# Performance work log

Hardware: AMD Instinct MI355X
Metric: run time of the kernel (lower is better)

## Reference

```python
import jax, jax.numpy as jnp
import numpy as np

KH, KW = 3, 3      # kernel_size
SH, SW = 1, 1      # stride
MINVAL, MAXVAL = -0.45, -0.15


def setup_inputs() -> dict:
    key = jax.random.key(0)
    kx, kw = jax.random.split(key)
    x = jax.random.normal(kx, (16, 128, 128, 16), dtype=jnp.float32)  # NHWC
    W = jax.random.uniform(kw, (KH, KW, 16, 32), minval=MINVAL, maxval=MAXVAL,
                           dtype=jnp.float32)  # [kh, kw, C_in, filters]
    return {"x": x, "W": W}


def _dilation(x, W):
    # Max-plus sliding-window 'convolution' (VALID padding):
    # out[b,i,j,f] = max_{di,dj,c} x[b, i*SH+di, j*SW+dj, c] + W[di,dj,c,f]
    kh, kw, C, F = W.shape
    B, H, Wd, _ = x.shape
    Hout = (H - kh) // SH + 1
    Wout = (Wd - kw) // SW + 1
    out = jnp.full((B, Hout, Wout, F), -jnp.inf, dtype=x.dtype)
    for di in range(kh):          # small fixed loop over kernel offsets
        for dj in range(kw):
            xs = x[:, di:di + Hout * SH:SH, dj:dj + Wout * SW:SW, :]  # [B,Hout,Wout,C]
            # add W for this offset, reduce max over input channels
            out = jnp.maximum(out, jnp.max(xs[..., :, None] + W[di, dj], axis=3))
    return out


def reference(x, W):
    # erosion(x) = -dilation(-x)
    return -_dilation(-x, W)
```

## Files before the change

kernel.cpp:

```cpp
#include <hip/hip_runtime.h>
#include <math.h>


#define TI 21

typedef _Float16 h2 __attribute__((ext_vector_type(2)));

__device__ __forceinline__ h2 hmin2(h2 a, h2 b) {
    return __builtin_elementwise_min(a, b);
}

__device__ __forceinline__ h2 pkrtz(float a, float b) {
    auto r = __builtin_amdgcn_cvt_pkrtz(a, b);
    return *reinterpret_cast<h2*>(&r);
}

__device__ __forceinline__ h2 rowmin(const h2* hx, const h2 w[3][4]) {
    h2 t[12];
#pragma unroll
    for (int dj = 0; dj < 3; ++dj)
#pragma unroll
        for (int q = 0; q < 4; ++q)
            t[dj * 4 + q] = hx[dj * 4 + q] - w[dj][q];
#pragma unroll
    for (int k = 0; k < 6; ++k) t[k] = hmin2(t[k], t[k + 6]);
    t[0] = hmin2(t[0], t[3]);
    t[1] = hmin2(t[1], t[4]);
    t[2] = hmin2(t[2], t[5]);
    return hmin2(hmin2(t[0], t[1]), t[2]);
}

__global__ __launch_bounds__(256) void erosion_kernel(
    const float* __restrict__ x, const float* __restrict__ Wt,
    float* __restrict__ out)
{
    const int tid = threadIdx.x;
    const int f  = tid & 31;
    const int ch = (tid >> 5) & 1;
    const int jt = tid >> 6;
    const int b  = blockIdx.z;
    const int i0 = blockIdx.y * TI;
    int j = blockIdx.x * 4 + jt;
    const bool jvalid = (j < 126);
    if (!jvalid) j = 125;

    h2 wh[3][3][4];
#pragma unroll
    for (int di = 0; di < 3; ++di)
#pragma unroll
        for (int dj = 0; dj < 3; ++dj)
#pragma unroll
            for (int q = 0; q < 4; ++q) {
                int p = di * 3 + dj;
                float a = Wt[(p * 16 + ch * 8 + 2 * q) * 32 + f];
                float c = Wt[(p * 16 + ch * 8 + 2 * q + 1) * 32 + f];
                wh[di][dj][q] = pkrtz(a, c);
            }

    const float* xb = x + ((size_t)b * 128 * 128 + (size_t)j) * 16 + ch * 8;
    float* op = out + (((size_t)b * 126 + i0) * 126 + j) * 32 + f;

    const _Float16 HINF = (_Float16)__builtin_huge_valf();
    h2 accB = {HINF, HINF};
    h2 accC = {HINF, HINF};

#pragma unroll 1
    for (int r = 0; r < TI + 2; ++r) {
        const float* xr = xb + (size_t)(i0 + r) * 2048;
        h2 hx[12];
#pragma unroll
        for (int dj = 0; dj < 3; ++dj) {
            float4 lo = *reinterpret_cast<const float4*>(xr + dj * 16);
            float4 hi = *reinterpret_cast<const float4*>(xr + dj * 16 + 4);
            hx[dj * 4 + 0] = pkrtz(lo.x, lo.y);
            hx[dj * 4 + 1] = pkrtz(lo.z, lo.w);
            hx[dj * 4 + 2] = pkrtz(hi.x, hi.y);
            hx[dj * 4 + 3] = pkrtz(hi.z, hi.w);
        }

        h2 n0 = rowmin(hx, wh[0]);
        h2 n1 = rowmin(hx, wh[1]);
        h2 n2 = rowmin(hx, wh[2]);

        h2 fin2 = hmin2(accC, n2);
        accC = hmin2(accB, n1);
        accB = n0;

        if (r >= 2) {
            float v = fminf((float)fin2[0], (float)fin2[1]);
            v = fminf(v, __shfl_xor(v, 32));
            if (jvalid && ch == 0)
                op[(size_t)(r - 2) * (126 * 32)] = v;
        }
    }
}

extern "C" void kernel_launch(void* const* d_in, const int* in_sizes, int n_in,
                              void* d_out, int out_size, void* d_ws, size_t ws_size,
                              hipStream_t stream) {
    const float* x  = (const float*)d_in[0];
    const float* Wt = (const float*)d_in[1];
    float* out = (float*)d_out;

    dim3 grid(32, 6, 16);
    dim3 block(256);
    erosion_kernel<<<grid, block, 0, stream>>>(x, Wt, out);
}
```

Before: 129.6 us.

## Pre-convert input to fp16 in workspace before the erosion kernel

Adds a conversion kernel that writes x as fp16 into the workspace, and an erosion kernel that reads fp16 rows, which halves the bytes loaded per row and removes the per-load conversions. The main loop is unrolled by 2 in both kernels, and the final lane reduction is done in fp16 before widening. The cost is an extra launch plus a full pass that reads x and writes the fp16 copy, and the fast path runs only if the workspace is large enough.

```diff
diff --git a/kernel.cpp b/kernel.cpp
--- a/kernel.cpp
+++ b/kernel.cpp
@@ -28,6 +28,81 @@
     t[1] = hmin2(t[1], t[4]);
     t[2] = hmin2(t[2], t[5]);
     return hmin2(hmin2(t[0], t[1]), t[2]);
+}
+
+__global__ __launch_bounds__(256) void cvt_kernel(const float* __restrict__ x,
+                                                  _Float16* __restrict__ xh) {
+    int idx = (blockIdx.x * 256 + threadIdx.x) * 8;
+    float4 a = *reinterpret_cast<const float4*>(x + idx);
+    float4 b = *reinterpret_cast<const float4*>(x + idx + 4);
+    h2 o[4] = { pkrtz(a.x, a.y), pkrtz(a.z, a.w), pkrtz(b.x, b.y), pkrtz(b.z, b.w) };
+    *reinterpret_cast<float4*>(xh + idx) = *reinterpret_cast<float4*>(o);
+}
+
+__global__ __launch_bounds__(256) void erosion_h_kernel(
+    const _Float16* __restrict__ xh, const float* __restrict__ Wt,
+    float* __restrict__ out)
+{
+    const int tid = threadIdx.x;
+    const int f  = tid & 31;
+    const int ch = (tid >> 5) & 1;
+    const int jt = tid >> 6;
+    const int b  = blockIdx.z;
+    const int i0 = blockIdx.y * TI;
+    int j = blockIdx.x * 4 + jt;
+    const bool jvalid = (j < 126);
+    if (!jvalid) j = 125;
+
+    h2 wh[3][3][4];
+#pragma unroll
+    for (int di = 0; di < 3; ++di)
+#pragma unroll
+        for (int dj = 0; dj < 3; ++dj)
+#pragma unroll
+            for (int q = 0; q < 4; ++q) {
+                int p = di * 3 + dj;
+                float a = Wt[(p * 16 + ch * 8 + 2 * q) * 32 + f];
+                float c = Wt[(p * 16 + ch * 8 + 2 * q + 1) * 32 + f];
+                wh[di][dj][q] = pkrtz(a, c);
+            }
+
+    const _Float16* xb = xh + ((size_t)b * 128 * 128 + (size_t)j) * 16 + ch * 8;
+    float* op = out + (((size_t)b * 126 + i0) * 126 + j) * 32 + f;
+
+    const _Float16 HINF = (_Float16)__builtin_huge_valf();
+    h2 accB = {HINF, HINF};
+    h2 accC = {HINF, HINF};
+
+#pragma unroll 2
+    for (int r = 0; r < TI + 2; ++r) {
+        const _Float16* xr = xb + (size_t)(i0 + r) * 2048;
+        h2 hx[12];
+#pragma unroll
+        for (int dj = 0; dj < 3; ++dj) {
+            float4 raw = *reinterpret_cast<const float4*>(xr + dj * 16);
+            const h2* p = reinterpret_cast<const h2*>(&raw);
+            hx[dj * 4 + 0] = p[0];
+            hx[dj * 4 + 1] = p[1];
+            hx[dj * 4 + 2] = p[2];
+            hx[dj * 4 + 3] = p[3];
+        }
+
+        h2 n0 = rowmin(hx, wh[0]);
+        h2 n1 = rowmin(hx, wh[1]);
+        h2 n2 = rowmin(hx, wh[2]);
+
+        h2 fin2 = hmin2(accC, n2);
+        accC = hmin2(accB, n1);
+        accB = n0;
+
+        if (r >= 2) {
+            _Float16 vm = fin2[0] < fin2[1] ? fin2[0] : fin2[1];
+            float v = (float)vm;
+            v = fminf(v, __shfl_xor(v, 32));
+            if (jvalid && ch == 0)
+                op[(size_t)(r - 2) * (126 * 32)] = v;
+        }
+    }
 }
 
 __global__ __launch_bounds__(256) void erosion_kernel(
@@ -64,7 +139,7 @@
     h2 accB = {HINF, HINF};
     h2 accC = {HINF, HINF};
 
-#pragma unroll 1
+#pragma unroll 2
     for (int r = 0; r < TI + 2; ++r) {
         const float* xr = xb + (size_t)(i0 + r) * 2048;
         h2 hx[12];
@@ -87,7 +162,8 @@
         accB = n0;
 
         if (r >= 2) {
-            float v = fminf((float)fin2[0], (float)fin2[1]);
+            _Float16 vm = fin2[0] < fin2[1] ? fin2[0] : fin2[1];
+            float v = (float)vm;
             v = fminf(v, __shfl_xor(v, 32));
             if (jvalid && ch == 0)
                 op[(size_t)(r - 2) * (126 * 32)] = v;
@@ -102,7 +178,15 @@
     const float* Wt = (const float*)d_in[1];
     float* out = (float*)d_out;
 
+    const size_t xelems = (size_t)16 * 128 * 128 * 16;
     dim3 grid(32, 6, 16);
     dim3 block(256);
-    erosion_kernel<<<grid, block, 0, stream>>>(x, Wt, out);
+
+    if (ws_size >= xelems * sizeof(_Float16)) {
+        _Float16* xh = (_Float16*)d_ws;
+        cvt_kernel<<<dim3(xelems / (256 * 8)), block, 0, stream>>>(x, xh);
+        erosion_h_kernel<<<grid, block, 0, stream>>>(xh, Wt, out);
+    } else {
+        erosion_kernel<<<grid, block, 0, stream>>>(x, Wt, out);
+    }
 }
```

Measured after the change: 118.5 us. 8.5% less time.

## Stage input tile into LDS as fp16 and double rows per block

Applied to the files above, without the earlier changes.

Each block now cooperatively loads its input rows and six columns into shared memory, converting to packed fp16 once, instead of every thread re-reading fp32 from global memory and converting per row. The row tile doubles so the grid halves, and the main loop is peeled and unrolled with a half-precision min before the shuffle. This removes redundant global loads and conversions across the 32 filter lanes, at the cost of a barrier, LDS usage, and fewer blocks in flight.

```diff
diff --git a/kernel.cpp b/kernel.cpp
--- a/kernel.cpp
+++ b/kernel.cpp
@@ -2,7 +2,9 @@
 #include <math.h>
 
 
-#define TI 21
+#define TI 42
+#define TROWS (TI + 2)
+#define LROW 64
 
 typedef _Float16 h2 __attribute__((ext_vector_type(2)));
 
@@ -34,15 +36,36 @@
     const float* __restrict__ x, const float* __restrict__ Wt,
     float* __restrict__ out)
 {
+    __shared__ _Float16 lds[2 * TROWS * LROW];
+
     const int tid = threadIdx.x;
     const int f  = tid & 31;
     const int ch = (tid >> 5) & 1;
     const int jt = tid >> 6;
     const int b  = blockIdx.z;
     const int i0 = blockIdx.y * TI;
-    int j = blockIdx.x * 4 + jt;
-    const bool jvalid = (j < 126);
-    if (!jvalid) j = 125;
+    const int jb = blockIdx.x * 4;
+    const int j  = jb + jt;
+    const bool writer = (j < 126) && (ch == 0);
+
+    {
+        const float* xg = x + (size_t)b * (128 * 128 * 16);
+        for (int t = tid; t < TROWS * 12; t += 256) {
+            int r   = t / 12;
+            int k   = t % 12;
+            int cc  = k >> 1;
+            int ch2 = k & 1;
+            int col = min(jb + cc, 127);
+            const float* src = xg + ((size_t)(i0 + r) * 128 + col) * 16 + ch2 * 8;
+            float4 lo = *reinterpret_cast<const float4*>(src);
+            float4 hi = *reinterpret_cast<const float4*>(src + 4);
+            h2 o[4] = { pkrtz(lo.x, lo.y), pkrtz(lo.z, lo.w),
+                        pkrtz(hi.x, hi.y), pkrtz(hi.z, hi.w) };
+            *reinterpret_cast<float4*>(
+                &lds[ch2 * (TROWS * LROW) + r * LROW + cc * 8]) =
+                *reinterpret_cast<float4*>(o);
+        }
+    }
 
     h2 wh[3][3][4];
 #pragma unroll
@@ -57,25 +80,25 @@
                 wh[di][dj][q] = pkrtz(a, c);
             }
 
-    const float* xb = x + ((size_t)b * 128 * 128 + (size_t)j) * 16 + ch * 8;
+    __syncthreads();
+
+    const _Float16* lb = &lds[ch * (TROWS * LROW) + jt * 8];
     float* op = out + (((size_t)b * 126 + i0) * 126 + j) * 32 + f;
 
     const _Float16 HINF = (_Float16)__builtin_huge_valf();
     h2 accB = {HINF, HINF};
     h2 accC = {HINF, HINF};
 
-#pragma unroll 1
-    for (int r = 0; r < TI + 2; ++r) {
-        const float* xr = xb + (size_t)(i0 + r) * 2048;
+    auto body = [&](int r, bool do_store) {
         h2 hx[12];
 #pragma unroll
         for (int dj = 0; dj < 3; ++dj) {
-            float4 lo = *reinterpret_cast<const float4*>(xr + dj * 16);
-            float4 hi = *reinterpret_cast<const float4*>(xr + dj * 16 + 4);
-            hx[dj * 4 + 0] = pkrtz(lo.x, lo.y);
-            hx[dj * 4 + 1] = pkrtz(lo.z, lo.w);
-            hx[dj * 4 + 2] = pkrtz(hi.x, hi.y);
-            hx[dj * 4 + 3] = pkrtz(hi.z, hi.w);
+            float4 raw = *reinterpret_cast<const float4*>(lb + r * LROW + dj * 8);
+            const h2* p = reinterpret_cast<const h2*>(&raw);
+            hx[dj * 4 + 0] = p[0];
+            hx[dj * 4 + 1] = p[1];
+            hx[dj * 4 + 2] = p[2];
+            hx[dj * 4 + 3] = p[3];
         }
 
         h2 n0 = rowmin(hx, wh[0]);
@@ -86,13 +109,20 @@
         accC = hmin2(accB, n1);
         accB = n0;
 
-        if (r >= 2) {
-            float v = fminf((float)fin2[0], (float)fin2[1]);
+        if (do_store) {
+            _Float16 vm = fin2[0] < fin2[1] ? fin2[0] : fin2[1];
+            float v = (float)vm;
             v = fminf(v, __shfl_xor(v, 32));
-            if (jvalid && ch == 0)
+            if (writer)
                 op[(size_t)(r - 2) * (126 * 32)] = v;
         }
-    }
+    };
+
+    body(0, false);
+    body(1, false);
+#pragma unroll 3
+    for (int r = 2; r < TROWS; ++r)
+        body(r, true);
 }
 
 extern "C" void kernel_launch(void* const* d_in, const int* in_sizes, int n_in,
@@ -102,7 +132,7 @@
     const float* Wt = (const float*)d_in[1];
     float* out = (float*)d_out;
 
-    dim3 grid(32, 6, 16);
+    dim3 grid(32, 3, 16);
     dim3 block(256);
     erosion_kernel<<<grid, block, 0, stream>>>(x, Wt, out);
 }
```

After: 113.6 us. 1.14x faster.
